# Optimization experiments

Hardware: AMD Instinct MI355X
Metric: run time of the kernel (lower is better)

Reference implementation:

```python
import jax, jax.numpy as jnp
import numpy as np

# Domain bounds and training nu-range (from init_kwargs)
X_MIN, X_MAX = -1.0, 1.0
Y_MIN, Y_MAX = -1.0, 1.0
T_MIN, T_MAX = 0.0, 1.0
NU_MIN, NU_MAX = 0.01, 0.1

LAYERS = [4, 256, 256, 256, 256, 2]
N = 16384  # collocation points


def setup_inputs() -> dict:
    key = jax.random.key(0)
    ks = jax.random.split(key, 4 + 2 * (len(LAYERS) - 1))
    inp = {
        'x': jax.random.uniform(ks[0], (N, 1), minval=X_MIN, maxval=X_MAX, dtype=jnp.float32),
        'y': jax.random.uniform(ks[1], (N, 1), minval=Y_MIN, maxval=Y_MAX, dtype=jnp.float32),
        't': jax.random.uniform(ks[2], (N, 1), minval=T_MIN, maxval=T_MAX, dtype=jnp.float32),
        'nu': jax.random.uniform(ks[3], (N, 1), minval=NU_MIN, maxval=NU_MAX, dtype=jnp.float32),
    }
    # glorot_normal weights, zero biases (keras Dense defaults)
    for i in range(len(LAYERS) - 1):
        fan_in, fan_out = LAYERS[i], LAYERS[i + 1]
        std = (2.0 / (fan_in + fan_out)) ** 0.5
        inp[f'W{i}'] = std * jax.random.normal(ks[4 + 2 * i], (fan_in, fan_out), dtype=jnp.float32)
        inp[f'b{i}'] = jnp.zeros((fan_out,), dtype=jnp.float32)
    return inp


def _net(pt, nu, params):
    """MLP forward for a single point. pt: (3,) = (x, y, t); nu: scalar. Returns (2,) = (u, v)."""
    x, y, t = pt[0], pt[1], pt[2]
    h = jnp.stack([
        2.0 * (x - X_MIN) / (X_MAX - X_MIN) - 1.0,
        2.0 * (y - Y_MIN) / (Y_MAX - Y_MIN) - 1.0,
        2.0 * (t - T_MIN) / (T_MAX - T_MIN) - 1.0,
        2.0 * (nu - NU_MIN) / (NU_MAX - NU_MIN) - 1.0,
    ])
    for W, b in params[:-1]:
        z = h @ W + b
        h = z * jax.nn.sigmoid(z)  # swish
    W, b = params[-1]
    return h @ W + b


def _residual_point(pt, nu, params):
    """Burgers PDE residual (f_u, f_v) at one collocation point via nested forward-mode AD."""
    f = lambda p: _net(p, nu, params)
    uv = f(pt)                          # (2,)
    J = jax.jacfwd(f)(pt)               # (2,3): d(u,v)/d(x,y,t)
    H = jax.jacfwd(jax.jacfwd(f))(pt)   # (2,3,3)
    u, v = uv[0], uv[1]
    u_x, u_y, u_t = J[0, 0], J[0, 1], J[0, 2]
    v_x, v_y, v_t = J[1, 0], J[1, 1], J[1, 2]
    u_xx, u_yy = H[0, 0, 0], H[0, 1, 1]
    v_xx, v_yy = H[1, 0, 0], H[1, 1, 1]
    f_u = u_t + u * u_x + v * u_y - nu * (u_xx + u_yy)
    f_v = v_t + u * v_x + v * v_y - nu * (v_xx + v_yy)
    return jnp.stack([f_u, f_v])


def reference(x, y, t, nu, W0, b0, W1, b1, W2, b2, W3, b3, W4, b4):
    params = [(W0, b0), (W1, b1), (W2, b2), (W3, b3), (W4, b4)]
    pts = jnp.concatenate([x, y, t], axis=1)  # (N, 3)
    res = jax.vmap(lambda p, n: _residual_point(p, n, params))(pts, nu[:, 0])
    return res  # (N, 2) = [f_u, f_v]
```

## Files before the change

### kernel.cpp

```cpp
#include <hip/hip_runtime.h>

typedef _Float16 f16;
typedef _Float16 v8hf __attribute__((ext_vector_type(8)));
typedef _Float16 v4hf __attribute__((ext_vector_type(4)));
typedef _Float16 v2hf __attribute__((ext_vector_type(2)));
typedef float    v4f  __attribute__((ext_vector_type(4)));

#define NPTS 16384
#define PTS  8
#define NLAYER_ELEMS 65536

__device__ __forceinline__ int swz(int m, int j) {
    return m * 256 + ((((j >> 3) ^ (m & 7)) << 3) | (j & 7));
}

__device__ __forceinline__ uint32_t pk_lo(float x0, float x1) {
    return __builtin_amdgcn_perm(__float_as_uint(x1), __float_as_uint(x0), 0x05040100u);
}
__device__ __forceinline__ uint32_t pk_hi(float x0, float x1) {
    return __builtin_amdgcn_perm(__float_as_uint(x1), __float_as_uint(x0), 0x07060302u);
}
__device__ __forceinline__ float up0(uint32_t lo, uint32_t hi) {
    return __uint_as_float(__builtin_amdgcn_perm(hi, lo, 0x05040100u));
}
__device__ __forceinline__ float up1(uint32_t lo, uint32_t hi) {
    return __uint_as_float(__builtin_amdgcn_perm(hi, lo, 0x07060302u));
}

__global__ void pack_weights(const float* __restrict__ W1, const float* __restrict__ W2,
                             const float* __restrict__ W3, f16* __restrict__ bh,
                             f16* __restrict__ bl) {
    const int b = blockIdx.x;
    const int L = b >> 5, r = b & 31, ks = r >> 2, i = r & 3;
    const int n = threadIdx.x;
    const float* W = (L == 0) ? W1 : (L == 1) ? W2 : W3;
    f16 h[8], l[8];
    #pragma unroll
    for (int j = 0; j < 8; ++j) {
        float w = W[(ks * 32 + i * 8 + j) * 256 + n];
        f16 hh = (f16)w;
        h[j] = hh;
        l[j] = (f16)(w - (float)hh);
    }
    size_t off = (size_t)L * NLAYER_ELEMS + (size_t)(ks * 256 + n) * 32 + (size_t)i * 8;
    *(v8hf*)(bh + off) = *(v8hf*)(h);
    *(v8hf*)(bl + off) = *(v8hf*)(l);
}

__global__ __launch_bounds__(256, 3) void pinn_burgers_kernel(
    const float* __restrict__ gx, const float* __restrict__ gy,
    const float* __restrict__ gt, const float* __restrict__ gnu,
    const float* __restrict__ W0, const float* __restrict__ b0,
    const float* __restrict__ b1, const float* __restrict__ b2,
    const float* __restrict__ b3,
    const float* __restrict__ W4, const float* __restrict__ b4,
    const f16* __restrict__ bh, const f16* __restrict__ bl,
    float* __restrict__ out)
{
    __shared__ f16 Ah[48 * 256];
    __shared__ f16 Al[48 * 256];
    __shared__ float red[PTS][12];
    __shared__ float pin[4][PTS];

    const int tid  = threadIdx.x;
    const int lane = tid & 63;
    const int wv   = tid >> 6;
    const int ln   = lane & 15;
    const int quad = lane >> 4;
    const int lnx  = ln & 7;
    const int p0   = blockIdx.x * PTS;

    if (tid < 4 * PTS) {
        int c = tid >> 3, p = tid & 7;
        const float* src = (c == 0) ? gx : (c == 1) ? gy : (c == 2) ? gt : gnu;
        pin[c][p] = src[p0 + p];
    }
    __syncthreads();

    const int pa    = lane >> 3;
    const int jb    = lane & 7;
    const int jbase = wv * 64 + jb * 8;

    auto store_split = [&](const float (&A)[8], int c) {
        v8hf hh, ll;
        #pragma unroll
        for (int e = 0; e < 8; ++e) {
            f16 hv = (f16)A[e];
            hh[e] = hv;
            ll[e] = (f16)(A[e] - (float)hv);
        }
        int idx = swz(c * PTS + pa, jbase);
        *(v8hf*)&Ah[idx] = hh;
        *(v8hf*)&Al[idx] = ll;
    };
    auto store_raw = [&](const float (&A)[8], int c) {
        uint4 lo, hi;
        lo.x = pk_lo(A[0], A[1]); lo.y = pk_lo(A[2], A[3]);
        lo.z = pk_lo(A[4], A[5]); lo.w = pk_lo(A[6], A[7]);
        hi.x = pk_hi(A[0], A[1]); hi.y = pk_hi(A[2], A[3]);
        hi.z = pk_hi(A[4], A[5]); hi.w = pk_hi(A[6], A[7]);
        int idx = swz(c * PTS + pa, jbase);
        *(uint4*)&Ah[idx] = lo;
        *(uint4*)&Al[idx] = hi;
    };

    {
        v4f w0v[2], w1v[2], w2v[2], w3v[2], bbv[2];
        #pragma unroll
        for (int h = 0; h < 2; ++h) {
            w0v[h] = *(const v4f*)(W0 +   0 + jbase + 4 * h);
            w1v[h] = *(const v4f*)(W0 + 256 + jbase + 4 * h);
            w2v[h] = *(const v4f*)(W0 + 512 + jbase + 4 * h);
            w3v[h] = *(const v4f*)(W0 + 768 + jbase + 4 * h);
            bbv[h] = *(const v4f*)(b0 + jbase + 4 * h);
        }
        float hx = pin[0][pa];
        float hy = pin[1][pa];
        float ht = 2.f * pin[2][pa] - 1.f;
        float hn = 2.f * (pin[3][pa] - 0.01f) * (1.f / 0.09f) - 1.f;
        float A0[8], A1[8], A2[8], A3[8], A4[8], A5[8];
        #pragma unroll
        for (int e = 0; e < 8; ++e) {
            float w0 = w0v[e >> 2][e & 3];
            float w1 = w1v[e >> 2][e & 3];
            float w2 = w2v[e >> 2][e & 3];
            float w3 = w3v[e >> 2][e & 3];
            float z  = hx * w0 + hy * w1 + ht * w2 + hn * w3 + bbv[e >> 2][e & 3];
            float zx = w0, zy = w1, zt = 2.f * w2;
            float s  = 1.f / (1.f + __expf(-z));
            float g1 = s * (1.f + z * (1.f - s));
            float g2 = s * (1.f - s) * (2.f + z * (1.f - 2.f * s));
            A0[e] = z * s;
            A1[e] = g1 * zx; A2[e] = g1 * zy; A3[e] = g1 * zt;
            A4[e] = g2 * zx * zx; A5[e] = g2 * zy * zy;
        }
        store_split(A0, 0); store_split(A1, 1); store_split(A2, 2);
        store_split(A3, 3); store_split(A4, 4); store_split(A5, 5);
    }
    __syncthreads();

    const float* bias_ptr[3] = { b1, b2, b3 };
    for (int L = 0; L < 3; ++L) {
        const f16* __restrict__ bhL = bh + (size_t)L * NLAYER_ELEMS;
        const f16* __restrict__ blL = bl + (size_t)L * NLAYER_ELEMS;
        const float* __restrict__ bv = bias_ptr[L];

        v4f acc[4][3];
        #pragma unroll
        for (int t = 0; t < 4; ++t)
            #pragma unroll
            for (int mt = 0; mt < 3; ++mt)
                acc[t][mt] = (v4f){0.f, 0.f, 0.f, 0.f};

        #pragma unroll 2
        for (int ks = 0; ks < 8; ++ks) {
            const int cb = (((4 * ks + quad) ^ lnx) << 3);
            v8hf a_h[3], a_l[3];
            #pragma unroll
            for (int mt = 0; mt < 3; ++mt) {
                const int rb = (mt * 16 + ln) * 256 + cb;
                a_h[mt] = *(const v8hf*)&Ah[rb];
                a_l[mt] = *(const v8hf*)&Al[rb];
            }
            v8hf w_h[4], w_l[4];
            #pragma unroll
            for (int t = 0; t < 4; ++t) {
                int n = wv * 64 + t * 16 + ln;
                size_t o = (size_t)(ks * 256 + n) * 32 + quad * 8;
                w_h[t] = *(const v8hf*)(bhL + o);
                w_l[t] = *(const v8hf*)(blL + o);
            }
            #pragma unroll
            for (int t = 0; t < 4; ++t)
                #pragma unroll
                for (int mt = 0; mt < 3; ++mt) {
                    acc[t][mt] = __builtin_amdgcn_mfma_f32_16x16x32_f16(w_h[t], a_h[mt], acc[t][mt], 0, 0, 0);
                    acc[t][mt] = __builtin_amdgcn_mfma_f32_16x16x32_f16(w_h[t], a_l[mt], acc[t][mt], 0, 0, 0);
                    acc[t][mt] = __builtin_amdgcn_mfma_f32_16x16x32_f16(w_l[t], a_h[mt], acc[t][mt], 0, 0, 0);
                }
        }
        __syncthreads();

        #pragma unroll
        for (int t = 0; t < 4; ++t)
            #pragma unroll
            for (int mt = 0; mt < 3; ++mt) {
                v4f a = acc[t][mt];
                int nb = wv * 64 + t * 16 + quad * 4;
                int m  = mt * 16 + ln;
                if (mt == 0 && ln < PTS) {
                    const float4 bq = *(const float4*)(bv + nb);
                    a[0] += bq.x; a[1] += bq.y; a[2] += bq.z; a[3] += bq.w;
                }
                int idx = swz(m, nb);
                uint2 lo, hi;
                lo.x = pk_lo(a[0], a[1]); lo.y = pk_lo(a[2], a[3]);
                hi.x = pk_hi(a[0], a[1]); hi.y = pk_hi(a[2], a[3]);
                *(uint2*)&Ah[idx] = lo;
                *(uint2*)&Al[idx] = hi;
            }

        {
            float z0[8], z1[8], z2[8], z3[8], z4[8], z5[8];
            auto load_z = [&](float (&Z)[8], int c) {
                int idx = swz(c * PTS + pa, jbase);
                uint4 lo = *(const uint4*)&Ah[idx];
                uint4 hi = *(const uint4*)&Al[idx];
                Z[0] = up0(lo.x, hi.x); Z[1] = up1(lo.x, hi.x);
                Z[2] = up0(lo.y, hi.y); Z[3] = up1(lo.y, hi.y);
                Z[4] = up0(lo.z, hi.z); Z[5] = up1(lo.z, hi.z);
                Z[6] = up0(lo.w, hi.w); Z[7] = up1(lo.w, hi.w);
            };
            load_z(z0, 0); load_z(z1, 1); load_z(z2, 2);
            load_z(z3, 3); load_z(z4, 4); load_z(z5, 5);

            float A0[8], g1[8], g2[8];
            #pragma unroll
            for (int e = 0; e < 8; ++e) {
                float zz = z0[e];
                float s  = 1.f / (1.f + __expf(-zz));
                A0[e] = zz * s;
                g1[e] = s * (1.f + zz * (1.f - s));
                g2[e] = s * (1.f - s) * (2.f + zz * (1.f - 2.f * s));
            }
            float A1[8], A2[8], A3[8], A4[8], A5[8];
            #pragma unroll
            for (int e = 0; e < 8; ++e) {
                A1[e] = g1[e] * z1[e];
                A2[e] = g1[e] * z2[e];
                A3[e] = g1[e] * z3[e];
                A4[e] = g2[e] * z1[e] * z1[e] + g1[e] * z4[e];
                A5[e] = g2[e] * z2[e] * z2[e] + g1[e] * z5[e];
            }
            if (L < 2) {
                store_split(A0, 0); store_split(A1, 1); store_split(A2, 2);
                store_split(A3, 3); store_split(A4, 4); store_split(A5, 5);
            } else {
                store_raw(A0, 0); store_raw(A1, 1); store_raw(A2, 2);
                store_raw(A3, 3); store_raw(A4, 4); store_raw(A5, 5);
            }
        }
        __syncthreads();
    }

    #pragma unroll
    for (int d = 0; d < 24; ++d) {
        int D  = wv * 24 + d;
        int p  = D / 12;
        int rm = D % 12;
        int c  = rm >> 1;
        int o  = rm & 1;
        int m  = c * PTS + p;
        int k0 = lane * 4;
        int idx = swz(m, k0);
        uint2 lo = *(const uint2*)&Ah[idx];
        uint2 hi = *(const uint2*)&Al[idx];
        float h0 = up0(lo.x, hi.x), h1 = up1(lo.x, hi.x);
        float h2 = up0(lo.y, hi.y), h3 = up1(lo.y, hi.y);
        float partial = h0 * W4[(k0 + 0) * 2 + o] + h1 * W4[(k0 + 1) * 2 + o]
                      + h2 * W4[(k0 + 2) * 2 + o] + h3 * W4[(k0 + 3) * 2 + o];
        #pragma unroll
        for (int off = 32; off > 0; off >>= 1)
            partial += __shfl_down(partial, off);
        if (lane == 0)
            red[p][rm] = partial + ((c == 0) ? b4[o] : 0.f);
    }
    __syncthreads();

    if (tid < PTS) {
        int p = tid;
        float u   = red[p][0],  v   = red[p][1];
        float ux  = red[p][2],  vx  = red[p][3];
        float uy  = red[p][4],  vy  = red[p][5];
        float ut  = red[p][6],  vt  = red[p][7];
        float uxx = red[p][8],  vxx = red[p][9];
        float uyy = red[p][10], vyy = red[p][11];
        float nuv = pin[3][p];
        float fu = ut + u * ux + v * uy - nuv * (uxx + uyy);
        float fv = vt + u * vx + v * vy - nuv * (vxx + vyy);
        out[(p0 + p) * 2 + 0] = fu;
        out[(p0 + p) * 2 + 1] = fv;
    }
}

extern "C" void kernel_launch(void* const* d_in, const int* in_sizes, int n_in,
                              void* d_out, int out_size, void* d_ws, size_t ws_size,
                              hipStream_t stream) {
    const float* x  = (const float*)d_in[0];
    const float* y  = (const float*)d_in[1];
    const float* t  = (const float*)d_in[2];
    const float* nu = (const float*)d_in[3];
    const float* W0 = (const float*)d_in[4];
    const float* b0 = (const float*)d_in[5];
    const float* W1 = (const float*)d_in[6];
    const float* b1 = (const float*)d_in[7];
    const float* W2 = (const float*)d_in[8];
    const float* b2 = (const float*)d_in[9];
    const float* W3 = (const float*)d_in[10];
    const float* b3 = (const float*)d_in[11];
    const float* W4 = (const float*)d_in[12];
    const float* b4 = (const float*)d_in[13];
    float* o = (float*)d_out;

    f16* bh = (f16*)d_ws;
    f16* bl = bh + 3 * (size_t)NLAYER_ELEMS;

    hipLaunchKernelGGL(pack_weights, dim3(96), dim3(256), 0, stream, W1, W2, W3, bh, bl);
    hipLaunchKernelGGL(pinn_burgers_kernel, dim3(NPTS / PTS), dim3(256), 0, stream,
                       x, y, t, nu, W0, b0, b1, b2, b3, W4, b4, bh, bl, o);
}
```

Before: 214.1 us.

## Double block size to 512 threads, halving per-wave output columns

The main kernel now runs 8 waves per block instead of 4. Each wave owns 32 output neurons instead of 64, and the per-thread layer-0 and activation work drops from 8 to 4 elements. Each wave also handles one point's final reduction. The aim is more waves in flight to hide global weight loads and LDS latency, at lower accumulator register pressure. The cost is that the same A tiles are read from LDS by twice as many waves, and the MFMA work per wave between barriers is halved.

```diff
diff --git a/kernel.cpp b/kernel.cpp
--- a/kernel.cpp
+++ b/kernel.cpp
@@ -47,7 +47,7 @@
     *(v8hf*)(bl + off) = *(v8hf*)(l);
 }
 
-__global__ __launch_bounds__(256, 3) void pinn_burgers_kernel(
+__global__ __launch_bounds__(512, 6) void pinn_burgers_kernel(
     const float* __restrict__ gx, const float* __restrict__ gy,
     const float* __restrict__ gt, const float* __restrict__ gnu,
     const float* __restrict__ W0, const float* __restrict__ b0,
@@ -78,54 +78,45 @@
     __syncthreads();
 
     const int pa    = lane >> 3;
-    const int jb    = lane & 7;
-    const int jbase = wv * 64 + jb * 8;
-
-    auto store_split = [&](const float (&A)[8], int c) {
-        v8hf hh, ll;
-        #pragma unroll
-        for (int e = 0; e < 8; ++e) {
+    const int jh    = lane & 7;
+    const int jbase = wv * 32 + jh * 4;
+
+    auto store_split = [&](const float (&A)[4], int c) {
+        v4hf hh, ll;
+        #pragma unroll
+        for (int e = 0; e < 4; ++e) {
             f16 hv = (f16)A[e];
             hh[e] = hv;
             ll[e] = (f16)(A[e] - (float)hv);
         }
         int idx = swz(c * PTS + pa, jbase);
-        *(v8hf*)&Ah[idx] = hh;
-        *(v8hf*)&Al[idx] = ll;
+        *(v4hf*)&Ah[idx] = hh;
+        *(v4hf*)&Al[idx] = ll;
     };
-    auto store_raw = [&](const float (&A)[8], int c) {
-        uint4 lo, hi;
+    auto store_raw = [&](const float (&A)[4], int c) {
+        uint2 lo, hi;
         lo.x = pk_lo(A[0], A[1]); lo.y = pk_lo(A[2], A[3]);
-        lo.z = pk_lo(A[4], A[5]); lo.w = pk_lo(A[6], A[7]);
         hi.x = pk_hi(A[0], A[1]); hi.y = pk_hi(A[2], A[3]);
-        hi.z = pk_hi(A[4], A[5]); hi.w = pk_hi(A[6], A[7]);
         int idx = swz(c * PTS + pa, jbase);
-        *(uint4*)&Ah[idx] = lo;
-        *(uint4*)&Al[idx] = hi;
+        *(uint2*)&Ah[idx] = lo;
+        *(uint2*)&Al[idx] = hi;
     };
 
     {
-        v4f w0v[2], w1v[2], w2v[2], w3v[2], bbv[2];
-        #pragma unroll
-        for (int h = 0; h < 2; ++h) {
-            w0v[h] = *(const v4f*)(W0 +   0 + jbase + 4 * h);
-            w1v[h] = *(const v4f*)(W0 + 256 + jbase + 4 * h);
-            w2v[h] = *(const v4f*)(W0 + 512 + jbase + 4 * h);
-            w3v[h] = *(const v4f*)(W0 + 768 + jbase + 4 * h);
-            bbv[h] = *(const v4f*)(b0 + jbase + 4 * h);
-        }
+        v4f w0v = *(const v4f*)(W0 +   0 + jbase);
+        v4f w1v = *(const v4f*)(W0 + 256 + jbase);
+        v4f w2v = *(const v4f*)(W0 + 512 + jbase);
+        v4f w3v = *(const v4f*)(W0 + 768 + jbase);
+        v4f bbv = *(const v4f*)(b0 + jbase);
         float hx = pin[0][pa];
         float hy = pin[1][pa];
         float ht = 2.f * pin[2][pa] - 1.f;
         float hn = 2.f * (pin[3][pa] - 0.01f) * (1.f / 0.09f) - 1.f;
-        float A0[8], A1[8], A2[8], A3[8], A4[8], A5[8];
-        #pragma unroll
-        for (int e = 0; e < 8; ++e) {
-            float w0 = w0v[e >> 2][e & 3];
-            float w1 = w1v[e >> 2][e & 3];
-            float w2 = w2v[e >> 2][e & 3];
-            float w3 = w3v[e >> 2][e & 3];
-            float z  = hx * w0 + hy * w1 + ht * w2 + hn * w3 + bbv[e >> 2][e & 3];
+        float A0[4], A1[4], A2[4], A3[4], A4[4], A5[4];
+        #pragma unroll
+        for (int e = 0; e < 4; ++e) {
+            float w0 = w0v[e], w1 = w1v[e], w2 = w2v[e], w3 = w3v[e];
+            float z  = hx * w0 + hy * w1 + ht * w2 + hn * w3 + bbv[e];
             float zx = w0, zy = w1, zt = 2.f * w2;
             float s  = 1.f / (1.f + __expf(-z));
             float g1 = s * (1.f + z * (1.f - s));
@@ -145,9 +136,9 @@
         const f16* __restrict__ blL = bl + (size_t)L * NLAYER_ELEMS;
         const float* __restrict__ bv = bias_ptr[L];
 
-        v4f acc[4][3];
-        #pragma unroll
-        for (int t = 0; t < 4; ++t)
+        v4f acc[2][3];
+        #pragma unroll
+        for (int t = 0; t < 2; ++t)
             #pragma unroll
             for (int mt = 0; mt < 3; ++mt)
                 acc[t][mt] = (v4f){0.f, 0.f, 0.f, 0.f};
@@ -162,16 +153,16 @@
                 a_h[mt] = *(const v8hf*)&Ah[rb];
                 a_l[mt] = *(const v8hf*)&Al[rb];
             }
-            v8hf w_h[4], w_l[4];
-            #pragma unroll
-            for (int t = 0; t < 4; ++t) {
-                int n = wv * 64 + t * 16 + ln;
+            v8hf w_h[2], w_l[2];
+            #pragma unroll
+            for (int t = 0; t < 2; ++t) {
+                int n = wv * 32 + t * 16 + ln;
                 size_t o = (size_t)(ks * 256 + n) * 32 + quad * 8;
                 w_h[t] = *(const v8hf*)(bhL + o);
                 w_l[t] = *(const v8hf*)(blL + o);
             }
             #pragma unroll
-            for (int t = 0; t < 4; ++t)
+            for (int t = 0; t < 2; ++t)
                 #pragma unroll
                 for (int mt = 0; mt < 3; ++mt) {
                     acc[t][mt] = __builtin_amdgcn_mfma_f32_16x16x32_f16(w_h[t], a_h[mt], acc[t][mt], 0, 0, 0);
@@ -182,11 +173,11 @@
         __syncthreads();
 
         #pragma unroll
-        for (int t = 0; t < 4; ++t)
+        for (int t = 0; t < 2; ++t)
             #pragma unroll
             for (int mt = 0; mt < 3; ++mt) {
                 v4f a = acc[t][mt];
-                int nb = wv * 64 + t * 16 + quad * 4;
+                int nb = wv * 32 + t * 16 + quad * 4;
                 int m  = mt * 16 + ln;
                 if (mt == 0 && ln < PTS) {
                     const float4 bq = *(const float4*)(bv + nb);
@@ -201,31 +192,29 @@
             }
 
         {
-            float z0[8], z1[8], z2[8], z3[8], z4[8], z5[8];
-            auto load_z = [&](float (&Z)[8], int c) {
+            float z0[4], z1[4], z2[4], z3[4], z4[4], z5[4];
+            auto load_z = [&](float (&Z)[4], int c) {
                 int idx = swz(c * PTS + pa, jbase);
-                uint4 lo = *(const uint4*)&Ah[idx];
-                uint4 hi = *(const uint4*)&Al[idx];
+                uint2 lo = *(const uint2*)&Ah[idx];
+                uint2 hi = *(const uint2*)&Al[idx];
                 Z[0] = up0(lo.x, hi.x); Z[1] = up1(lo.x, hi.x);
                 Z[2] = up0(lo.y, hi.y); Z[3] = up1(lo.y, hi.y);
-                Z[4] = up0(lo.z, hi.z); Z[5] = up1(lo.z, hi.z);
-                Z[6] = up0(lo.w, hi.w); Z[7] = up1(lo.w, hi.w);
             };
             load_z(z0, 0); load_z(z1, 1); load_z(z2, 2);
             load_z(z3, 3); load_z(z4, 4); load_z(z5, 5);
 
-            float A0[8], g1[8], g2[8];
-            #pragma unroll
-            for (int e = 0; e < 8; ++e) {
+            float A0[4], g1[4], g2[4];
+            #pragma unroll
+            for (int e = 0; e < 4; ++e) {
                 float zz = z0[e];
                 float s  = 1.f / (1.f + __expf(-zz));
                 A0[e] = zz * s;
                 g1[e] = s * (1.f + zz * (1.f - s));
                 g2[e] = s * (1.f - s) * (2.f + zz * (1.f - 2.f * s));
             }
-            float A1[8], A2[8], A3[8], A4[8], A5[8];
-            #pragma unroll
-            for (int e = 0; e < 8; ++e) {
+            float A1[4], A2[4], A3[4], A4[4], A5[4];
+            #pragma unroll
+            for (int e = 0; e < 4; ++e) {
                 A1[e] = g1[e] * z1[e];
                 A2[e] = g1[e] * z2[e];
                 A3[e] = g1[e] * z3[e];
@@ -244,12 +233,10 @@
     }
 
     #pragma unroll
-    for (int d = 0; d < 24; ++d) {
-        int D  = wv * 24 + d;
-        int p  = D / 12;
-        int rm = D % 12;
-        int c  = rm >> 1;
-        int o  = rm & 1;
+    for (int d = 0; d < 12; ++d) {
+        int p  = wv;
+        int c  = d >> 1;
+        int o  = d & 1;
         int m  = c * PTS + p;
         int k0 = lane * 4;
         int idx = swz(m, k0);
@@ -263,7 +250,7 @@
         for (int off = 32; off > 0; off >>= 1)
             partial += __shfl_down(partial, off);
         if (lane == 0)
-            red[p][rm] = partial + ((c == 0) ? b4[o] : 0.f);
+            red[p][d] = partial + ((c == 0) ? b4[o] : 0.f);
     }
     __syncthreads();
 
@@ -306,6 +293,6 @@
     f16* bl = bh + 3 * (size_t)NLAYER_ELEMS;
 
     hipLaunchKernelGGL(pack_weights, dim3(96), dim3(256), 0, stream, W1, W2, W3, bh, bl);
-    hipLaunchKernelGGL(pinn_burgers_kernel, dim3(NPTS / PTS), dim3(256), 0, stream,
+    hipLaunchKernelGGL(pinn_burgers_kernel, dim3(NPTS / PTS), dim3(512), 0, stream,
                        x, y, t, nu, W0, b0, b1, b2, b3, W4, b4, bh, bl, o);
 }
```

After: 216.2 us. About the same (+1.0%).

## Apply swish and derivative propagation directly on MFMA accumulators via lane shuffles

Applied to the files above, without the earlier changes.

Instead of writing pre-activations to shared memory, syncing, reloading them in a different layout and then applying the swish and its derivative chain, each wave now computes the activation terms directly from its MFMA accumulator registers. It uses xor-8 lane shuffles to pair the value rows with the derivative rows. This removes one shared-memory round trip and a barrier per hidden layer. In exchange it adds cross-lane shuffles, holds more results in registers across the barrier, and relies on a careful mapping of the row layout (z0/zx/zy/zt/zxx/zyy across the 16-row tiles).

```diff
diff --git a/kernel.cpp b/kernel.cpp
--- a/kernel.cpp
+++ b/kernel.cpp
@@ -69,6 +69,7 @@
     const int quad = lane >> 4;
     const int lnx  = ln & 7;
     const int p0   = blockIdx.x * PTS;
+    const bool hiL = (ln & 8) != 0;
 
     if (tid < 4 * PTS) {
         int c = tid >> 3, p = tid & 7;
@@ -81,7 +82,7 @@
     const int jb    = lane & 7;
     const int jbase = wv * 64 + jb * 8;
 
-    auto store_split = [&](const float (&A)[8], int c) {
+    auto store_split0 = [&](const float (&A)[8], int c) {
         v8hf hh, ll;
         #pragma unroll
         for (int e = 0; e < 8; ++e) {
@@ -92,16 +93,6 @@
         int idx = swz(c * PTS + pa, jbase);
         *(v8hf*)&Ah[idx] = hh;
         *(v8hf*)&Al[idx] = ll;
-    };
-    auto store_raw = [&](const float (&A)[8], int c) {
-        uint4 lo, hi;
-        lo.x = pk_lo(A[0], A[1]); lo.y = pk_lo(A[2], A[3]);
-        lo.z = pk_lo(A[4], A[5]); lo.w = pk_lo(A[6], A[7]);
-        hi.x = pk_hi(A[0], A[1]); hi.y = pk_hi(A[2], A[3]);
-        hi.z = pk_hi(A[4], A[5]); hi.w = pk_hi(A[6], A[7]);
-        int idx = swz(c * PTS + pa, jbase);
-        *(uint4*)&Ah[idx] = lo;
-        *(uint4*)&Al[idx] = hi;
     };
 
     {
@@ -134,8 +125,8 @@
             A1[e] = g1 * zx; A2[e] = g1 * zy; A3[e] = g1 * zt;
             A4[e] = g2 * zx * zx; A5[e] = g2 * zy * zy;
         }
-        store_split(A0, 0); store_split(A1, 1); store_split(A2, 2);
-        store_split(A3, 3); store_split(A4, 4); store_split(A5, 5);
+        store_split0(A0, 0); store_split0(A1, 1); store_split0(A2, 2);
+        store_split0(A3, 3); store_split0(A4, 4); store_split0(A5, 5);
     }
     __syncthreads();
 
@@ -179,67 +170,71 @@
                     acc[t][mt] = __builtin_amdgcn_mfma_f32_16x16x32_f16(w_l[t], a_h[mt], acc[t][mt], 0, 0, 0);
                 }
         }
+
+        v4hf hhv[4][3], llv[4][3];
+        uint2 lov[4][3], hiv[4][3];
+        #pragma unroll
+        for (int t = 0; t < 4; ++t) {
+            const float4 bq = *(const float4*)(bv + wv * 64 + t * 16 + quad * 4);
+            const float bqa[4] = { bq.x, bq.y, bq.z, bq.w };
+            v4f o0 = acc[t][0], o1 = acc[t][1], o2 = acc[t][2];
+            v4f s0, s1;
+            #pragma unroll
+            for (int e = 0; e < 4; ++e) {
+                s0[e] = __shfl_xor(o0[e], 8);
+                s1[e] = __shfl_xor(o1[e], 8);
+            }
+            v4f r0v, r1v, r2v;
+            #pragma unroll
+            for (int e = 0; e < 4; ++e) {
+                float z0 = (hiL ? s0[e] : o0[e]) + bqa[e];
+                float x  = hiL ? s1[e] : s0[e];
+                float s  = 1.f / (1.f + __expf(-z0));
+                float g1 = s * (1.f + z0 * (1.f - s));
+                float g2 = s * (1.f - s) * (2.f + z0 * (1.f - 2.f * s));
+                r0v[e] = hiL ? (g1 * o0[e]) : (z0 * s);
+                r1v[e] = g1 * o1[e];
+                r2v[e] = g2 * x * x + g1 * o2[e];
+            }
+            v4f rr[3] = { r0v, r1v, r2v };
+            if (L < 2) {
+                #pragma unroll
+                for (int mt = 0; mt < 3; ++mt) {
+                    v4hf hh, ll;
+                    #pragma unroll
+                    for (int e = 0; e < 4; ++e) {
+                        f16 hv = (f16)rr[mt][e];
+                        hh[e] = hv;
+                        ll[e] = (f16)(rr[mt][e] - (float)hv);
+                    }
+                    hhv[t][mt] = hh;
+                    llv[t][mt] = ll;
+                }
+            } else {
+                #pragma unroll
+                for (int mt = 0; mt < 3; ++mt) {
+                    lov[t][mt] = (uint2){ pk_lo(rr[mt][0], rr[mt][1]), pk_lo(rr[mt][2], rr[mt][3]) };
+                    hiv[t][mt] = (uint2){ pk_hi(rr[mt][0], rr[mt][1]), pk_hi(rr[mt][2], rr[mt][3]) };
+                }
+            }
+        }
+
         __syncthreads();
 
         #pragma unroll
         for (int t = 0; t < 4; ++t)
             #pragma unroll
             for (int mt = 0; mt < 3; ++mt) {
-                v4f a = acc[t][mt];
-                int nb = wv * 64 + t * 16 + quad * 4;
-                int m  = mt * 16 + ln;
-                if (mt == 0 && ln < PTS) {
-                    const float4 bq = *(const float4*)(bv + nb);
-                    a[0] += bq.x; a[1] += bq.y; a[2] += bq.z; a[3] += bq.w;
+                const int nb  = wv * 64 + t * 16 + quad * 4;
+                const int idx = swz(mt * 16 + ln, nb);
+                if (L < 2) {
+                    *(v4hf*)&Ah[idx] = hhv[t][mt];
+                    *(v4hf*)&Al[idx] = llv[t][mt];
+                } else {
+                    *(uint2*)&Ah[idx] = lov[t][mt];
+                    *(uint2*)&Al[idx] = hiv[t][mt];
                 }
-                int idx = swz(m, nb);
-                uint2 lo, hi;
-                lo.x = pk_lo(a[0], a[1]); lo.y = pk_lo(a[2], a[3]);
-                hi.x = pk_hi(a[0], a[1]); hi.y = pk_hi(a[2], a[3]);
-                *(uint2*)&Ah[idx] = lo;
-                *(uint2*)&Al[idx] = hi;
-            }
-
-        {
-            float z0[8], z1[8], z2[8], z3[8], z4[8], z5[8];
-            auto load_z = [&](float (&Z)[8], int c) {
-                int idx = swz(c * PTS + pa, jbase);
-                uint4 lo = *(const uint4*)&Ah[idx];
-                uint4 hi = *(const uint4*)&Al[idx];
-                Z[0] = up0(lo.x, hi.x); Z[1] = up1(lo.x, hi.x);
-                Z[2] = up0(lo.y, hi.y); Z[3] = up1(lo.y, hi.y);
-                Z[4] = up0(lo.z, hi.z); Z[5] = up1(lo.z, hi.z);
-                Z[6] = up0(lo.w, hi.w); Z[7] = up1(lo.w, hi.w);
-            };
-            load_z(z0, 0); load_z(z1, 1); load_z(z2, 2);
-            load_z(z3, 3); load_z(z4, 4); load_z(z5, 5);
-
-            float A0[8], g1[8], g2[8];
-            #pragma unroll
-            for (int e = 0; e < 8; ++e) {
-                float zz = z0[e];
-                float s  = 1.f / (1.f + __expf(-zz));
-                A0[e] = zz * s;
-                g1[e] = s * (1.f + zz * (1.f - s));
-                g2[e] = s * (1.f - s) * (2.f + zz * (1.f - 2.f * s));
-            }
-            float A1[8], A2[8], A3[8], A4[8], A5[8];
-            #pragma unroll
-            for (int e = 0; e < 8; ++e) {
-                A1[e] = g1[e] * z1[e];
-                A2[e] = g1[e] * z2[e];
-                A3[e] = g1[e] * z3[e];
-                A4[e] = g2[e] * z1[e] * z1[e] + g1[e] * z4[e];
-                A5[e] = g2[e] * z2[e] * z2[e] + g1[e] * z5[e];
-            }
-            if (L < 2) {
-                store_split(A0, 0); store_split(A1, 1); store_split(A2, 2);
-                store_split(A3, 3); store_split(A4, 4); store_split(A5, 5);
-            } else {
-                store_raw(A0, 0); store_raw(A1, 1); store_raw(A2, 2);
-                store_raw(A3, 3); store_raw(A4, 4); store_raw(A5, 5);
-            }
-        }
+            }
         __syncthreads();
     }
 
```

Result: slower. 298.1 us (+39.2%).

## Double-buffer weight loads across k-steps and layers, hoist W4/b4 loads

Applied to the files above, without the earlier changes.

Adds a register double-buffer for the global hi/lo f16 weight fragments so the loads for the next k-step, and the first k-step of the next layer, are issued before the current step's MFMAs. The layer and k loops are now fully unrolled so the buffer selection resolves at compile time. Accumulator packing moves ahead of the barrier, leaving only LDS stores after it, and the final-layer W4/b4 values are loaded once into registers at kernel start. The aim is to hide global load latency behind MFMA work, at the cost of more VGPR pressure and code size, which could lower occupancy.

```diff
diff --git a/kernel.cpp b/kernel.cpp
--- a/kernel.cpp
+++ b/kernel.cpp
@@ -70,6 +70,11 @@
     const int lnx  = ln & 7;
     const int p0   = blockIdx.x * PTS;
 
+    const int k0w = lane * 4;
+    const v4f w4a = *(const v4f*)(W4 + k0w * 2);
+    const v4f w4b = *(const v4f*)(W4 + k0w * 2 + 4);
+    const float b40 = b4[0], b41 = b4[1];
+
     if (tid < 4 * PTS) {
         int c = tid >> 3, p = tid & 7;
         const float* src = (c == 0) ? gx : (c == 1) ? gy : (c == 2) ? gt : gnu;
@@ -80,6 +85,19 @@
     const int pa    = lane >> 3;
     const int jb    = lane & 7;
     const int jbase = wv * 64 + jb * 8;
+
+    auto ldw = [&](int Lidx, int ks, v8hf (&WH)[4], v8hf (&WL)[4]) {
+        const f16* __restrict__ bhL = bh + (size_t)Lidx * NLAYER_ELEMS;
+        const f16* __restrict__ blL = bl + (size_t)Lidx * NLAYER_ELEMS;
+        #pragma unroll
+        for (int t = 0; t < 4; ++t) {
+            int n = wv * 64 + t * 16 + ln;
+            size_t o = (size_t)(ks * 256 + n) * 32 + quad * 8;
+            WH[t] = *(const v8hf*)(bhL + o);
+            WL[t] = *(const v8hf*)(blL + o);
+        }
+    };
+    v8hf wAh[4], wAl[4], wBh[4], wBl[4];
 
     auto store_split = [&](const float (&A)[8], int c) {
         v8hf hh, ll;
@@ -137,12 +155,12 @@
         store_split(A0, 0); store_split(A1, 1); store_split(A2, 2);
         store_split(A3, 3); store_split(A4, 4); store_split(A5, 5);
     }
+    ldw(0, 0, wAh, wAl);
     __syncthreads();
 
     const float* bias_ptr[3] = { b1, b2, b3 };
+    #pragma unroll
     for (int L = 0; L < 3; ++L) {
-        const f16* __restrict__ bhL = bh + (size_t)L * NLAYER_ELEMS;
-        const f16* __restrict__ blL = bl + (size_t)L * NLAYER_ELEMS;
         const float* __restrict__ bv = bias_ptr[L];
 
         v4f acc[4][3];
@@ -152,8 +170,12 @@
             for (int mt = 0; mt < 3; ++mt)
                 acc[t][mt] = (v4f){0.f, 0.f, 0.f, 0.f};
 
-        #pragma unroll 2
+        #pragma unroll
         for (int ks = 0; ks < 8; ++ks) {
+            if (ks < 7) {
+                if (ks & 1) ldw(L, ks + 1, wAh, wAl);
+                else        ldw(L, ks + 1, wBh, wBl);
+            }
             const int cb = (((4 * ks + quad) ^ lnx) << 3);
             v8hf a_h[3], a_l[3];
             #pragma unroll
@@ -162,43 +184,46 @@
                 a_h[mt] = *(const v8hf*)&Ah[rb];
                 a_l[mt] = *(const v8hf*)&Al[rb];
             }
-            v8hf w_h[4], w_l[4];
-            #pragma unroll
-            for (int t = 0; t < 4; ++t) {
-                int n = wv * 64 + t * 16 + ln;
-                size_t o = (size_t)(ks * 256 + n) * 32 + quad * 8;
-                w_h[t] = *(const v8hf*)(bhL + o);
-                w_l[t] = *(const v8hf*)(blL + o);
-            }
             #pragma unroll
             for (int t = 0; t < 4; ++t)
                 #pragma unroll
                 for (int mt = 0; mt < 3; ++mt) {
-                    acc[t][mt] = __builtin_amdgcn_mfma_f32_16x16x32_f16(w_h[t], a_h[mt], acc[t][mt], 0, 0, 0);
-                    acc[t][mt] = __builtin_amdgcn_mfma_f32_16x16x32_f16(w_h[t], a_l[mt], acc[t][mt], 0, 0, 0);
-                    acc[t][mt] = __builtin_amdgcn_mfma_f32_16x16x32_f16(w_l[t], a_h[mt], acc[t][mt], 0, 0, 0);
+                    const v8hf ch = (ks & 1) ? wBh[t] : wAh[t];
+                    const v8hf cl = (ks & 1) ? wBl[t] : wAl[t];
+                    acc[t][mt] = __builtin_amdgcn_mfma_f32_16x16x32_f16(ch, a_h[mt], acc[t][mt], 0, 0, 0);
+                    acc[t][mt] = __builtin_amdgcn_mfma_f32_16x16x32_f16(ch, a_l[mt], acc[t][mt], 0, 0, 0);
+                    acc[t][mt] = __builtin_amdgcn_mfma_f32_16x16x32_f16(cl, a_h[mt], acc[t][mt], 0, 0, 0);
                 }
         }
-        __syncthreads();
-
+
+        uint2 pkA[4][3], pkB[4][3];
         #pragma unroll
         for (int t = 0; t < 4; ++t)
             #pragma unroll
             for (int mt = 0; mt < 3; ++mt) {
                 v4f a = acc[t][mt];
                 int nb = wv * 64 + t * 16 + quad * 4;
-                int m  = mt * 16 + ln;
                 if (mt == 0 && ln < PTS) {
                     const float4 bq = *(const float4*)(bv + nb);
                     a[0] += bq.x; a[1] += bq.y; a[2] += bq.z; a[3] += bq.w;
                 }
-                int idx = swz(m, nb);
-                uint2 lo, hi;
-                lo.x = pk_lo(a[0], a[1]); lo.y = pk_lo(a[2], a[3]);
-                hi.x = pk_hi(a[0], a[1]); hi.y = pk_hi(a[2], a[3]);
-                *(uint2*)&Ah[idx] = lo;
-                *(uint2*)&Al[idx] = hi;
-            }
+                pkA[t][mt] = (uint2){ pk_lo(a[0], a[1]), pk_lo(a[2], a[3]) };
+                pkB[t][mt] = (uint2){ pk_hi(a[0], a[1]), pk_hi(a[2], a[3]) };
+            }
+
+        __syncthreads();
+
+        #pragma unroll
+        for (int t = 0; t < 4; ++t)
+            #pragma unroll
+            for (int mt = 0; mt < 3; ++mt) {
+                const int nb  = wv * 64 + t * 16 + quad * 4;
+                const int idx = swz(mt * 16 + ln, nb);
+                *(uint2*)&Ah[idx] = pkA[t][mt];
+                *(uint2*)&Al[idx] = pkB[t][mt];
+            }
+
+        if (L < 2) ldw(L + 1, 0, wAh, wAl);
 
         {
             float z0[8], z1[8], z2[8], z3[8], z4[8], z5[8];
@@ -251,19 +276,19 @@
         int c  = rm >> 1;
         int o  = rm & 1;
         int m  = c * PTS + p;
-        int k0 = lane * 4;
-        int idx = swz(m, k0);
+        int idx = swz(m, k0w);
         uint2 lo = *(const uint2*)&Ah[idx];
         uint2 hi = *(const uint2*)&Al[idx];
         float h0 = up0(lo.x, hi.x), h1 = up1(lo.x, hi.x);
         float h2 = up0(lo.y, hi.y), h3 = up1(lo.y, hi.y);
-        float partial = h0 * W4[(k0 + 0) * 2 + o] + h1 * W4[(k0 + 1) * 2 + o]
-                      + h2 * W4[(k0 + 2) * 2 + o] + h3 * W4[(k0 + 3) * 2 + o];
+        float partial = (o == 0)
+            ? (h0 * w4a[0] + h1 * w4a[2] + h2 * w4b[0] + h3 * w4b[2])
+            : (h0 * w4a[1] + h1 * w4a[3] + h2 * w4b[1] + h3 * w4b[3]);
         #pragma unroll
         for (int off = 32; off > 0; off >>= 1)
             partial += __shfl_down(partial, off);
         if (lane == 0)
-            red[p][rm] = partial + ((c == 0) ? b4[o] : 0.f);
+            red[p][rm] = partial + ((c == 0) ? ((o == 0) ? b40 : b41) : 0.f);
     }
     __syncthreads();
 
```

New measurement: 220.3 us. 1.03x slower.
